# Performance work log

Measured on AMD Instinct MI355X. Metric: run time of the kernel, lower is better.

The kernel has to match this reference:

```python
import jax, jax.numpy as jnp
import numpy as np
from jax import lax

BS = 64    # block size
NH = 8     # attention heads
L = 12     # layers
NEG = -1e9
EPS = 1e-12  # BigBird layer_norm_eps


def gelu_new(x):
    c = 0.7978845608028654  # sqrt(2/pi)
    return 0.5 * x * (1.0 + jnp.tanh(c * (x + 0.044715 * x * x * x)))


def layer_norm(x, s, b):
    m = jnp.mean(x, axis=-1, keepdims=True)
    v = jnp.var(x, axis=-1, keepdims=True)
    return (x - m) * lax.rsqrt(v + EPS) * s + b


def block_sparse_attn(q, k, v, mask, key_blocks):
    # q,k,v: [B,H,S,hd]; mask: [B,S] (1=keep); key_blocks: [nb-2, K] block ids
    B, H, S, hd = q.shape
    nb = S // BS
    nm = nb - 2
    K = key_blocks.shape[1]
    scale = 1.0 / np.sqrt(hd)
    qb = q.reshape(B, H, nb, BS, hd)
    kb = k.reshape(B, H, nb, BS, hd)
    vb = v.reshape(B, H, nb, BS, hd)
    mb = mask.reshape(B, nb, BS)
    # middle query blocks: attend to gathered global+window+random key blocks
    q_mid = qb[:, :, 1:-1]                                   # [B,H,nm,BS,hd]
    kg = kb[:, :, key_blocks]                                # [B,H,nm,K,BS,hd]
    vg = vb[:, :, key_blocks].reshape(B, H, nm, K * BS, hd)
    mg = mb[:, key_blocks].reshape(B, 1, nm, 1, K * BS)
    s_mid = jnp.einsum('bhnqd,bhnkzd->bhnqkz', q_mid, kg).reshape(B, H, nm, BS, K * BS)
    s_mid = s_mid * scale + NEG * (1.0 - mg)
    ctx_mid = jnp.einsum('bhnqk,bhnkd->bhnqd', jax.nn.softmax(s_mid, axis=-1), vg)
    # first/last query blocks are global: full attention rows
    q_edge = jnp.stack([qb[:, :, 0], qb[:, :, -1]], axis=2)  # [B,H,2,BS,hd]
    s_edge = jnp.einsum('bhnqd,bhkd->bhnqk', q_edge, k) * scale
    s_edge = s_edge + NEG * (1.0 - mask)[:, None, None, None, :]
    ctx_edge = jnp.einsum('bhnqk,bhkd->bhnqd', jax.nn.softmax(s_edge, axis=-1), v)
    ctx = jnp.concatenate([ctx_edge[:, :, :1], ctx_mid, ctx_edge[:, :, 1:]], axis=2)
    return ctx.reshape(B, H, S, hd)


def encoder_layer(x, p, mask, key_blocks):
    Wq, bq, Wk, bk, Wv, bv, Wo, bo, l1s, l1b, Wi_, bi_, Wo2_, bo2_, l2s, l2b = p
    B, S, Hm = x.shape
    hd = Hm // NH
    def heads(t):
        return t.reshape(B, S, NH, hd).transpose(0, 2, 1, 3)
    q = heads(x @ Wq + bq)
    k = heads(x @ Wk + bk)
    v = heads(x @ Wv + bv)
    ctx = block_sparse_attn(q, k, v, mask, key_blocks)
    ctx = ctx.transpose(0, 2, 1, 3).reshape(B, S, Hm)
    x = layer_norm(x + ctx @ Wo + bo, l1s, l1b)
    ff = gelu_new(x @ Wi_ + bi_) @ Wo2_ + bo2_
    return layer_norm(x + ff, l2s, l2b)


def forward(x, proj_w, proj_b, pos_emb, tok_emb, emb_ln_s, emb_ln_b, Wq, bq, Wk, bk, Wv, bv, Wo, bo, ln1_s, ln1_b, Wi, bi, Wo2, bo2, ln2_s, ln2_b, cw1, cb1, cw2, cb2, mask, key_blocks):
    h = x @ proj_w + proj_b                 # input projection to hidden 1536
    h = h + pos_emb[None] + tok_emb         # BigBird embeddings (token_type id 0)
    h = layer_norm(h, emb_ln_s, emb_ln_b)
    stack = (Wq, bq, Wk, bk, Wv, bv, Wo, bo, ln1_s, ln1_b, Wi, bi, Wo2, bo2, ln2_s, ln2_b)
    def body(carry, p):
        return encoder_layer(carry, p, mask, key_blocks), None
    h, _ = lax.scan(jax.checkpoint(body), h, stack)
    # replaced classifier head applied per token: Linear->ReLU->Linear
    return jnp.maximum(h @ cw1 + cb1, 0.0) @ cw2 + cb2


def setup_inputs():
    key = jax.random.key(0)
    ks = iter(jax.random.split(key, 64))
    def w(*shape):
        return jax.random.normal(next(ks), shape, jnp.float32) * 0.02
    B, S, DIN, H, FF, T = 1, 4096, 1280, 1536, 3072, 256
    nb = S // BS
    # deterministic random-block plan: per middle block, 3 random blocks
    # outside {global 0, global nb-1, window i-1..i+1}
    rng = np.random.RandomState(0)
    rows = []
    for i in range(1, nb - 1):
        fixed = [0, nb - 1, i - 1, i, i + 1]
        cand = np.setdiff1d(np.arange(nb), np.array(fixed))
        rows.append(fixed + list(rng.choice(cand, 3, replace=False)))
    key_blocks = jnp.asarray(np.array(rows, dtype=np.int32))
    z = jnp.zeros
    o = jnp.ones
    return dict(
        x=jax.random.normal(next(ks), (B, S, DIN), jnp.float32),
        proj_w=w(DIN, H), proj_b=z((H,)),
        pos_emb=w(S, H), tok_emb=w(H),
        emb_ln_s=o((H,)), emb_ln_b=z((H,)),
        Wq=w(L, H, H), bq=z((L, H)), Wk=w(L, H, H), bk=z((L, H)),
        Wv=w(L, H, H), bv=z((L, H)), Wo=w(L, H, H), bo=z((L, H)),
        ln1_s=o((L, H)), ln1_b=z((L, H)),
        Wi=w(L, H, FF), bi=z((L, FF)), Wo2=w(L, FF, H), bo2=z((L, H)),
        ln2_s=o((L, H)), ln2_b=z((L, H)),
        cw1=w(H, 512), cb1=z((512,)), cw2=w(512, T), cb2=z((T,)),
        attention_mask=jnp.ones((B, S), jnp.int32),
        key_blocks=key_blocks)


def reference(x, proj_w, proj_b, pos_emb, tok_emb, emb_ln_s, emb_ln_b, Wq, bq, Wk, bk, Wv, bv, Wo, bo, ln1_s, ln1_b, Wi, bi, Wo2, bo2, ln2_s, ln2_b, cw1, cb1, cw2, cb2, attention_mask, key_blocks):
    mask = attention_mask.astype(jnp.float32)
    return forward(x, proj_w, proj_b, pos_emb, tok_emb, emb_ln_s, emb_ln_b, Wq, bq, Wk, bk, Wv, bv, Wo, bo, ln1_s, ln1_b, Wi, bi, Wo2, bo2, ln2_s, ln2_b, cw1, cb1, cw2, cb2, mask, key_blocks)
```

## Files before the change

kernel.cpp:

```cpp
#include <hip/hip_runtime.h>

typedef unsigned short u16;
typedef unsigned int u32;
typedef __bf16 bf16x8 __attribute__((ext_vector_type(8)));
typedef float f32x4 __attribute__((ext_vector_type(4)));

#define SEQ 4096
#define HM 1536
#define QKVN 4608

__device__ inline u16 f2b(float f){
  u32 u = __builtin_bit_cast(u32, f);
  return (u16)((u + 0x7fffu + ((u>>16)&1u)) >> 16);
}
__device__ inline bf16x8 ld8(const u16* p){ return *reinterpret_cast<const bf16x8*>(p); }
__device__ inline void gload16(const void* g, void* l){
  __builtin_amdgcn_global_load_lds((const __attribute__((address_space(1))) void*)g,
                                   (__attribute__((address_space(3))) void*)l, 16, 0, 0);
}

__global__ void cvt_k(const float* __restrict__ in, u16* __restrict__ outp, int n4){
  int i = blockIdx.x*256 + threadIdx.x;
  if (i < n4){
    float4 f = reinterpret_cast<const float4*>(in)[i];
    ushort4 u; u.x=f2b(f.x); u.y=f2b(f.y); u.z=f2b(f.z); u.w=f2b(f.w);
    reinterpret_cast<ushort4*>(outp)[i] = u;
  }
}

__global__ void tconv(const float* __restrict__ W, u16* __restrict__ Wt, int K, int N){
  __shared__ float tile[32][33];
  int n0 = blockIdx.x*32, k0 = blockIdx.y*32;
  int tx = threadIdx.x, ty = threadIdx.y;
  #pragma unroll
  for (int i=0;i<4;i++){
    int kk = ty + i*8;
    tile[kk][tx] = W[(size_t)(k0+kk)*N + n0 + tx];
  }
  __syncthreads();
  #pragma unroll
  for (int i=0;i<4;i++){
    int nn = ty + i*8;
    Wt[(size_t)(n0+nn)*K + k0 + tx] = f2b(tile[tx][nn]);
  }
}

__global__ void tconv3(const float* __restrict__ W0, const float* __restrict__ W1,
                       const float* __restrict__ W2, u16* __restrict__ Wt){
  __shared__ float tile[32][33];
  const float* W = (blockIdx.z==0) ? W0 : (blockIdx.z==1 ? W1 : W2);
  u16* dst = Wt + (size_t)blockIdx.z*1536*1536;
  int n0 = blockIdx.x*32, k0 = blockIdx.y*32;
  int tx = threadIdx.x, ty = threadIdx.y;
  #pragma unroll
  for (int i=0;i<4;i++){
    int kk = ty + i*8;
    tile[kk][tx] = W[(size_t)(k0+kk)*1536 + n0 + tx];
  }
  __syncthreads();
  #pragma unroll
  for (int i=0;i<4;i++){
    int nn = ty + i*8;
    dst[(size_t)(n0+nn)*1536 + k0 + tx] = f2b(tile[tx][nn]);
  }
}

__global__ void vtrans_k(const u16* __restrict__ qkv, u16* __restrict__ vt){
  __shared__ u16 tile[32][33];
  int c0 = blockIdx.x*32, s0 = blockIdx.y*32;
  int tx = threadIdx.x, ty = threadIdx.y;
  #pragma unroll
  for (int i=0;i<4;i++)
    tile[ty+i*8][tx] = qkv[(size_t)(s0+ty+i*8)*QKVN + 3072 + c0 + tx];
  __syncthreads();
  #pragma unroll
  for (int i=0;i<4;i++)
    vt[(size_t)(c0+ty+i*8)*SEQ + s0 + tx] = tile[tx][ty+i*8];
}

__global__ void concat3_k(float* __restrict__ dst, const float* __restrict__ a,
                          const float* __restrict__ b, const float* __restrict__ c){
  int i = blockIdx.x*256 + threadIdx.x;
  if (i < 1536){ dst[i]=a[i]; dst[1536+i]=b[i]; dst[3072+i]=c[i]; }
}

template<int MODE>
__global__ __launch_bounds__(256) void gemm_k(
                       const u16* __restrict__ A, const u16* __restrict__ Bt,
                       const float* __restrict__ bias, const float* __restrict__ resid,
                       const float* __restrict__ pos, const float* __restrict__ tok,
                       u16* __restrict__ outB, float* __restrict__ outF,
                       int M, int N, int K){
  __shared__ __align__(16) u16 As[128*32];
  __shared__ __align__(16) u16 Bs[128*32];
  const int t = threadIdx.x;
  const int m0 = blockIdx.y*128, n0 = blockIdx.x*128;
  const int w = t>>6, l = t&63;
  const int wm = (w>>1)*64, wn = (w&1)*64;
  const int lr = l&15, lg = l>>4;
  const int srow = w*32 + (l>>2);
  const int scol = (l&3)*8;
  const u16* Ap = A  + (size_t)(m0 + srow)*K + scol;
  const u16* Bp = Bt + (size_t)(n0 + srow)*K + scol;
  f32x4 acc[4][4] = {};

  for (int k0 = 0; k0 < K; k0 += 32){
    #pragma unroll
    for (int i=0;i<2;i++){
      gload16(Ap + (size_t)i*16*K + k0, &As[(w*2+i)*512]);
      gload16(Bp + (size_t)i*16*K + k0, &Bs[(w*2+i)*512]);
    }
    __syncthreads();
    bf16x8 af[4], bfr[4];
    #pragma unroll
    for (int i=0;i<4;i++){
      af[i]  = ld8(&As[(wm + i*16 + lr)*32 + lg*8]);
      bfr[i] = ld8(&Bs[(wn + i*16 + lr)*32 + lg*8]);
    }
    #pragma unroll
    for (int i=0;i<4;i++)
      #pragma unroll
      for (int j=0;j<4;j++)
        acc[i][j] = __builtin_amdgcn_mfma_f32_16x16x32_bf16(af[i], bfr[j], acc[i][j], 0,0,0);
    __syncthreads();
  }

  #pragma unroll
  for (int i=0;i<4;i++){
    #pragma unroll
    for (int j=0;j<4;j++){
      int col = n0 + wn + j*16 + lr;
      float bv = bias[col];
      #pragma unroll
      for (int r2=0;r2<4;r2++){
        int row = m0 + wm + i*16 + lg*4 + r2;
        float v = acc[i][j][r2] + bv;
        size_t idx = (size_t)row*N + col;
        if (MODE==0) outB[idx] = f2b(v);
        else if (MODE==1) outF[idx] = v + resid[idx];
        else if (MODE==2){
          float g = 0.5f*v*(1.f + tanhf(0.7978845608028654f*(v + 0.044715f*v*v*v)));
          outB[idx] = f2b(g);
        }
        else if (MODE==3) outB[idx] = f2b(fmaxf(v, 0.f));
        else if (MODE==4) outF[idx] = v;
        else if (MODE==5) outF[idx] = v + pos[idx] + tok[col];
      }
    }
  }
}

__global__ void ln_k(const float* __restrict__ in, const float* __restrict__ g,
                     const float* __restrict__ bta, float* __restrict__ xf,
                     u16* __restrict__ xb){
  const int row = blockIdx.x, t = threadIdx.x;
  const float2* rp = reinterpret_cast<const float2*>(in + (size_t)row*HM);
  float2 v[3]; float s=0.f, s2=0.f;
  #pragma unroll
  for (int i=0;i<3;i++){
    v[i] = rp[t + i*256];
    s += v[i].x + v[i].y; s2 += v[i].x*v[i].x + v[i].y*v[i].y;
  }
  #pragma unroll
  for (int o=32;o;o>>=1){ s += __shfl_down(s,o,64); s2 += __shfl_down(s2,o,64); }
  __shared__ float red[8];
  if ((t&63)==0){ red[t>>6]=s; red[4+(t>>6)]=s2; }
  __syncthreads();
  s = red[0]+red[1]+red[2]+red[3]; s2 = red[4]+red[5]+red[6]+red[7];
  float mean = s*(1.f/1536.f);
  float var  = s2*(1.f/1536.f) - mean*mean;
  float inv  = rsqrtf(var + 1e-12f);
  float2* xfp = reinterpret_cast<float2*>(xf + (size_t)row*HM);
  u32*    xbp = reinterpret_cast<u32*>(xb + (size_t)row*HM);
  #pragma unroll
  for (int i=0;i<3;i++){
    int c2 = t + i*256;
    float2 gg = reinterpret_cast<const float2*>(g)[c2];
    float2 bb = reinterpret_cast<const float2*>(bta)[c2];
    float y0 = (v[i].x-mean)*inv*gg.x + bb.x;
    float y1 = (v[i].y-mean)*inv*gg.y + bb.y;
    xfp[c2] = make_float2(y0, y1);
    xbp[c2] = (u32)f2b(y0) | ((u32)f2b(y1) << 16);
  }
}

__device__ inline int sp_off(int row, int colu16){
  return row*256 + ((((colu16)*2) ^ ((row&7)<<4)) >> 1);
}

__global__ __launch_bounds__(256, 2) void attn_k(
    const u16* __restrict__ qkv, const u16* __restrict__ vt,
    const int* __restrict__ kblocks, const int* __restrict__ amask,
    u16* __restrict__ ctx, float* __restrict__ pO,
    float* __restrict__ pm, float* __restrict__ pl){
  __shared__ __align__(16) u16 sQ[64][200];
  __shared__ __align__(16) u16 sP[64*256];
  __shared__ float swm[4][64];
  __shared__ float swl[4][64];
  __shared__ float s_m[64];
  __shared__ float s_l[64];
  __shared__ float s_al[64];

  const int t = threadIdx.x, w = t>>6, l = t&63;
  const int lr = l&15, lg = l>>4;
  const int b = blockIdx.x;
  int h, qb, split;
  bool partial;
  if (b < 496){ h = b/62; qb = 1 + b%62; split = 0; partial = false; }
  else { int e = b-496; split = e&7; int idx = e>>3; h = idx>>1; qb = (idx&1)?63:0; partial = true; }

  {
    const u16* qg = qkv + (size_t)(qb*64)*QKVN + h*192;
    #pragma unroll
    for (int i=0;i<6;i++){
      int idx = t + i*256;
      int row = idx/24, c8 = idx%24;
      *reinterpret_cast<int4*>(&sQ[row][c8*8]) =
        *reinterpret_cast<const int4*>(qg + (size_t)row*QKVN + c8*8);
    }
  }
  if (t < 64){ s_m[t] = -3.0e38f; s_l[t] = 0.f; }
  __syncthreads();

  f32x4 accO[4][3] = {};
  const float scale = 0.07216878364870323f;

  for (int c = 0; c < 2; ++c){
    int kb4[4];
    #pragma unroll
    for (int idx=0;idx<4;idx++)
      kb4[idx] = partial ? (split*8 + c*4 + idx) : kblocks[(qb-1)*8 + c*4 + idx];
    const int kb = kb4[w];
    const u16* kp = qkv + (size_t)(kb*64)*QKVN + 1536 + h*192;
    f32x4 acc[4][4] = {};
    #pragma unroll
    for (int d0=0; d0<192; d0+=32){
      bf16x8 aq[4], bk_[4];
      #pragma unroll
      for (int i=0;i<4;i++)  aq[i]  = ld8(&sQ[i*16+lr][d0+lg*8]);
      #pragma unroll
      for (int jn=0;jn<4;jn++) bk_[jn] = ld8(kp + (size_t)(jn*16+lr)*QKVN + d0 + lg*8);
      #pragma unroll
      for (int i=0;i<4;i++)
        #pragma unroll
        for (int jn=0;jn<4;jn++)
          acc[i][jn] = __builtin_amdgcn_mfma_f32_16x16x32_bf16(aq[i], bk_[jn], acc[i][jn], 0,0,0);
    }
    bf16x8 bvx[8][3];
    #pragma unroll
    for (int ks=0; ks<8; ks++){
      const int sb = kb4[ks>>1]*64 + (ks&1)*32 + lg*8;
      #pragma unroll
      for (int jn=0;jn<3;jn++)
        bvx[ks][jn] = ld8(vt + (size_t)(h*192 + w*48 + jn*16 + lr)*SEQ + sb);
    }
    float mcol[4];
    #pragma unroll
    for (int jn=0;jn<4;jn++)
      mcol[jn] = -1e9f*(1.f - (float)amask[kb*64 + jn*16 + lr]);
    float rmax[4][4];
    #pragma unroll
    for (int i=0;i<4;i++)
      #pragma unroll
      for (int r2=0;r2<4;r2++){
        float mx = -3.0e38f;
        #pragma unroll
        for (int jn=0;jn<4;jn++){
          float sv = acc[i][jn][r2]*scale + mcol[jn];
          acc[i][jn][r2] = sv;
          mx = fmaxf(mx, sv);
        }
        #pragma unroll
        for (int o=1;o<16;o<<=1) mx = fmaxf(mx, __shfl_xor(mx, o, 64));
        rmax[i][r2] = mx;
      }
    if (lr == 0){
      #pragma unroll
      for (int i=0;i<4;i++)
        #pragma unroll
        for (int r2=0;r2<4;r2++)
          swm[w][i*16+lg*4+r2] = rmax[i][r2];
    }
    __syncthreads();
    if (t < 64){
      float mo = s_m[t];
      float mn = fmaxf(fmaxf(fmaxf(swm[0][t], swm[1][t]), fmaxf(swm[2][t], swm[3][t])), mo);
      s_al[t] = __expf(mo - mn);
      s_m[t]  = mn;
    }
    __syncthreads();
    #pragma unroll
    for (int i=0;i<4;i++)
      #pragma unroll
      for (int r2=0;r2<4;r2++){
        const int row = i*16 + lg*4 + r2;
        const float mrow = s_m[row];
        float ssum = 0.f;
        #pragma unroll
        for (int jn=0;jn<4;jn++){
          float p = __expf(acc[i][jn][r2] - mrow);
          ssum += p;
          sP[sp_off(row, w*64 + jn*16 + lr)] = f2b(p);
        }
        #pragma unroll
        for (int o=1;o<16;o<<=1) ssum += __shfl_xor(ssum, o, 64);
        if (lr == 0) swl[w][row] = ssum;
      }
    #pragma unroll
    for (int i=0;i<4;i++)
      #pragma unroll
      for (int r2=0;r2<4;r2++){
        float a = s_al[i*16+lg*4+r2];
        #pragma unroll
        for (int jn=0;jn<3;jn++) accO[i][jn][r2] *= a;
      }
    __syncthreads();
    if (t < 64)
      s_l[t] = s_l[t]*s_al[t] + swl[0][t]+swl[1][t]+swl[2][t]+swl[3][t];
    #pragma unroll
    for (int ks=0; ks<8; ks++){
      bf16x8 ap[4];
      #pragma unroll
      for (int i=0;i<4;i++) ap[i] = ld8(&sP[sp_off(i*16+lr, ks*32 + lg*8)]);
      #pragma unroll
      for (int i=0;i<4;i++)
        #pragma unroll
        for (int jn=0;jn<3;jn++)
          accO[i][jn] = __builtin_amdgcn_mfma_f32_16x16x32_bf16(ap[i], bvx[ks][jn], accO[i][jn], 0,0,0);
    }
  }
  __syncthreads();
  if (!partial){
    #pragma unroll
    for (int i=0;i<4;i++)
      #pragma unroll
      for (int r2=0;r2<4;r2++){
        const int row = i*16+lg*4+r2;
        const float inv = 1.f / s_l[row];
        #pragma unroll
        for (int jn=0;jn<3;jn++){
          const int col = h*192 + w*48 + jn*16 + lr;
          ctx[(size_t)(qb*64+row)*HM + col] = f2b(accO[i][jn][r2] * inv);
        }
      }
  } else {
    const int e = b - 496;
    #pragma unroll
    for (int i=0;i<4;i++)
      #pragma unroll
      for (int r2=0;r2<4;r2++){
        const int row = i*16+lg*4+r2;
        #pragma unroll
        for (int jn=0;jn<3;jn++){
          const int col = w*48 + jn*16 + lr;
          pO[((size_t)e*64 + row)*192 + col] = accO[i][jn][r2];
        }
      }
    if (t < 64){ pm[e*64 + t] = s_m[t]; pl[e*64 + t] = s_l[t]; }
  }
}

__global__ void attn_comb_k(const float* __restrict__ pO, const float* __restrict__ pm,
                            const float* __restrict__ pl, u16* __restrict__ ctx){
  const int b = blockIdx.x;
  const int h = b>>1, qb = (b&1)?63:0;
  const int t = threadIdx.x;
  __shared__ float sA[8][64];
  __shared__ float sInv[64];
  if (t < 64){
    float mv[8]; float M = -3.0e38f;
    #pragma unroll
    for (int s=0;s<8;s++){ mv[s] = pm[(b*8+s)*64 + t]; M = fmaxf(M, mv[s]); }
    float L = 0.f;
    #pragma unroll
    for (int s=0;s<8;s++){
      float a = __expf(mv[s]-M);
      sA[s][t] = a;
      L += pl[(b*8+s)*64 + t]*a;
    }
    sInv[t] = 1.f/L;
  }
  __syncthreads();
  #pragma unroll
  for (int i=0;i<48;i++){
    int idx = t + i*256;
    int row = idx/192, col = idx%192;
    float acc = 0.f;
    #pragma unroll
    for (int s=0;s<8;s++)
      acc += sA[s][row] * pO[((size_t)(b*8+s)*64 + row)*192 + col];
    ctx[(size_t)(qb*64+row)*HM + h*192 + col] = f2b(acc * sInv[row]);
  }
}

extern "C" void kernel_launch(void* const* d_in, const int* in_sizes, int n_in,
                              void* d_out, int out_size, void* d_ws, size_t ws_size,
                              hipStream_t stream){
  const float* x       = (const float*)d_in[0];
  const float* proj_w  = (const float*)d_in[1];
  const float* proj_b  = (const float*)d_in[2];
  const float* pos_emb = (const float*)d_in[3];
  const float* tok_emb = (const float*)d_in[4];
  const float* embs    = (const float*)d_in[5];
  const float* embb    = (const float*)d_in[6];
  const float* Wq  = (const float*)d_in[7];
  const float* bq  = (const float*)d_in[8];
  const float* Wk  = (const float*)d_in[9];
  const float* bk  = (const float*)d_in[10];
  const float* Wv  = (const float*)d_in[11];
  const float* bv  = (const float*)d_in[12];
  const float* Wo  = (const float*)d_in[13];
  const float* bo  = (const float*)d_in[14];
  const float* l1s = (const float*)d_in[15];
  const float* l1b = (const float*)d_in[16];
  const float* Wi  = (const float*)d_in[17];
  const float* bi  = (const float*)d_in[18];
  const float* Wo2 = (const float*)d_in[19];
  const float* bo2 = (const float*)d_in[20];
  const float* l2s = (const float*)d_in[21];
  const float* l2b = (const float*)d_in[22];
  const float* cw1 = (const float*)d_in[23];
  const float* cb1 = (const float*)d_in[24];
  const float* cw2 = (const float*)d_in[25];
  const float* cb2 = (const float*)d_in[26];
  const int* amask = (const int*)d_in[27];
  const int* kblk  = (const int*)d_in[28];
  float* out = (float*)d_out;

  char* base = (char*)d_ws;
  size_t off = 0;
  auto carve = [&](size_t bytes)->char*{
    char* p = base + off; off += (bytes + 255) & ~(size_t)255; return p;
  };
  float* xf32  = (float*)carve(4096ULL*1536*4);
  float* preln = (float*)carve(4096ULL*1536*4);
  u16*   xbf   = (u16*)  carve(4096ULL*1536*2);
  u16*   xinbf = (u16*)  carve(4096ULL*1280*2);
  u16*   qkv   = (u16*)  carve(4096ULL*4608*2);
  u16*   vt    = (u16*)  carve(1536ULL*4096*2);
  u16*   ctx   = (u16*)  carve(4096ULL*1536*2);
  u16*   ff1   = (u16*)  carve(4096ULL*3072*2);
  u16*   cls1  = (u16*)  carve(4096ULL*512*2);
  u16*   wt    = (u16*)  carve(4608ULL*1536*2);
  float* b3    = (float*)carve(4608ULL*4);
  float* pO    = (float*)carve(128ULL*64*192*4);
  float* pm    = (float*)carve(128ULL*64*4);
  float* pl    = (float*)carve(128ULL*64*4);
  if (off > ws_size) return;

  const dim3 tb32(32,8);

  cvt_k<<<5120, 256, 0, stream>>>(x, xinbf, 4096*1280/4);
  tconv<<<dim3(48,40), tb32, 0, stream>>>(proj_w, wt, 1280, 1536);
  gemm_k<5><<<dim3(12,32), 256, 0, stream>>>(xinbf, wt, proj_b, nullptr, pos_emb, tok_emb,
                                             nullptr, preln, 4096, 1536, 1280);
  ln_k<<<4096, 256, 0, stream>>>(preln, embs, embb, xf32, xbf);

  for (int l = 0; l < 12; ++l){
    const float* wq  = Wq  + (size_t)l*1536*1536;
    const float* wk  = Wk  + (size_t)l*1536*1536;
    const float* wv  = Wv  + (size_t)l*1536*1536;
    const float* wo  = Wo  + (size_t)l*1536*1536;
    const float* wi  = Wi  + (size_t)l*1536*3072;
    const float* wo2 = Wo2 + (size_t)l*3072*1536;
    const float* bql = bq  + (size_t)l*1536;
    const float* bkl = bk  + (size_t)l*1536;
    const float* bvl = bv  + (size_t)l*1536;
    const float* bol = bo  + (size_t)l*1536;
    const float* bil = bi  + (size_t)l*3072;
    const float* bo2l= bo2 + (size_t)l*1536;
    const float* g1  = l1s + (size_t)l*1536;
    const float* be1 = l1b + (size_t)l*1536;
    const float* g2  = l2s + (size_t)l*1536;
    const float* be2 = l2b + (size_t)l*1536;

    tconv3<<<dim3(48,48,3), tb32, 0, stream>>>(wq, wk, wv, wt);
    concat3_k<<<6, 256, 0, stream>>>(b3, bql, bkl, bvl);
    gemm_k<0><<<dim3(36,32), 256, 0, stream>>>(xbf, wt, b3, nullptr, nullptr, nullptr,
                                               qkv, nullptr, 4096, 4608, 1536);
    vtrans_k<<<dim3(48,128), tb32, 0, stream>>>(qkv, vt);

    attn_k<<<624, 256, 0, stream>>>(qkv, vt, kblk, amask, ctx, pO, pm, pl);
    attn_comb_k<<<16, 256, 0, stream>>>(pO, pm, pl, ctx);

    tconv<<<dim3(48,48), tb32, 0, stream>>>(wo, wt, 1536, 1536);
    gemm_k<1><<<dim3(12,32), 256, 0, stream>>>(ctx, wt, bol, xf32, nullptr, nullptr,
                                               nullptr, preln, 4096, 1536, 1536);
    ln_k<<<4096, 256, 0, stream>>>(preln, g1, be1, xf32, xbf);

    tconv<<<dim3(96,48), tb32, 0, stream>>>(wi, wt, 1536, 3072);
    gemm_k<2><<<dim3(24,32), 256, 0, stream>>>(xbf, wt, bil, nullptr, nullptr, nullptr,
                                               ff1, nullptr, 4096, 3072, 1536);
    tconv<<<dim3(48,96), tb32, 0, stream>>>(wo2, wt, 3072, 1536);
    gemm_k<1><<<dim3(12,32), 256, 0, stream>>>(ff1, wt, bo2l, xf32, nullptr, nullptr,
                                               nullptr, preln, 4096, 1536, 3072);
    ln_k<<<4096, 256, 0, stream>>>(preln, g2, be2, xf32, xbf);
  }

  tconv<<<dim3(16,48), tb32, 0, stream>>>(cw1, wt, 1536, 512);
  gemm_k<3><<<dim3(4,32), 256, 0, stream>>>(xbf, wt, cb1, nullptr, nullptr, nullptr,
                                            cls1, nullptr, 4096, 512, 1536);
  tconv<<<dim3(8,16), tb32, 0, stream>>>(cw2, wt, 512, 256);
  gemm_k<4><<<dim3(2,32), 256, 0, stream>>>(cls1, wt, cb2, nullptr, nullptr, nullptr,
                                            nullptr, out, 4096, 256, 512);

  (void)in_sizes; (void)n_in; (void)out_size;
}
```

Before: 6.104 ms.

## Fuse V transpose into QKV GEMM, move residual into LN, shrink attention LDS

The QKV GEMM epilogue now writes the V columns straight into the transposed vt buffer, so the separate vtrans kernel goes away. The residual add moves out of the output-projection GEMMs into the LayerNorm kernel, which reads a bf16 GEMM output plus the fp32 residual. This removes the fp32 preln buffer traffic but rounds the pre-residual sum to bf16. The attention kernel halves its P scratch in LDS and stages P in two halves with extra barriers so it can run 3 blocks per CU. V fragments are now loaded per k-step instead of being preloaded into registers.

```diff
diff --git a/kernel.cpp b/kernel.cpp
--- a/kernel.cpp
+++ b/kernel.cpp
@@ -13,6 +13,7 @@
   u32 u = __builtin_bit_cast(u32, f);
   return (u16)((u + 0x7fffu + ((u>>16)&1u)) >> 16);
 }
+__device__ inline float b2f(u16 h){ return __builtin_bit_cast(float, (u32)h << 16); }
 __device__ inline bf16x8 ld8(const u16* p){ return *reinterpret_cast<const bf16x8*>(p); }
 __device__ inline void gload16(const void* g, void* l){
   __builtin_amdgcn_global_load_lds((const __attribute__((address_space(1))) void*)g,
@@ -65,19 +66,6 @@
   }
 }
 
-__global__ void vtrans_k(const u16* __restrict__ qkv, u16* __restrict__ vt){
-  __shared__ u16 tile[32][33];
-  int c0 = blockIdx.x*32, s0 = blockIdx.y*32;
-  int tx = threadIdx.x, ty = threadIdx.y;
-  #pragma unroll
-  for (int i=0;i<4;i++)
-    tile[ty+i*8][tx] = qkv[(size_t)(s0+ty+i*8)*QKVN + 3072 + c0 + tx];
-  __syncthreads();
-  #pragma unroll
-  for (int i=0;i<4;i++)
-    vt[(size_t)(c0+ty+i*8)*SEQ + s0 + tx] = tile[tx][ty+i*8];
-}
-
 __global__ void concat3_k(float* __restrict__ dst, const float* __restrict__ a,
                           const float* __restrict__ b, const float* __restrict__ c){
   int i = blockIdx.x*256 + threadIdx.x;
@@ -87,8 +75,9 @@
 template<int MODE>
 __global__ __launch_bounds__(256) void gemm_k(
                        const u16* __restrict__ A, const u16* __restrict__ Bt,
-                       const float* __restrict__ bias, const float* __restrict__ resid,
+                       const float* __restrict__ bias,
                        const float* __restrict__ pos, const float* __restrict__ tok,
+                       u16* __restrict__ vtp,
                        u16* __restrict__ outB, float* __restrict__ outF,
                        int M, int N, int K){
   __shared__ __align__(16) u16 As[128*32];
@@ -131,13 +120,22 @@
     for (int j=0;j<4;j++){
       int col = n0 + wn + j*16 + lr;
       float bv = bias[col];
+      const int row0 = m0 + wm + i*16 + lg*4;
+      if (MODE==0 && col >= 3072){
+        ushort4 q;
+        q.x = f2b(acc[i][j][0] + bv);
+        q.y = f2b(acc[i][j][1] + bv);
+        q.z = f2b(acc[i][j][2] + bv);
+        q.w = f2b(acc[i][j][3] + bv);
+        *reinterpret_cast<ushort4*>(&vtp[(size_t)(col-3072)*SEQ + row0]) = q;
+        continue;
+      }
       #pragma unroll
       for (int r2=0;r2<4;r2++){
-        int row = m0 + wm + i*16 + lg*4 + r2;
+        int row = row0 + r2;
         float v = acc[i][j][r2] + bv;
         size_t idx = (size_t)row*N + col;
-        if (MODE==0) outB[idx] = f2b(v);
-        else if (MODE==1) outF[idx] = v + resid[idx];
+        if (MODE==0 || MODE==1) outB[idx] = f2b(v);
         else if (MODE==2){
           float g = 0.5f*v*(1.f + tanhf(0.7978845608028654f*(v + 0.044715f*v*v*v)));
           outB[idx] = f2b(g);
@@ -150,15 +148,22 @@
   }
 }
 
-__global__ void ln_k(const float* __restrict__ in, const float* __restrict__ g,
-                     const float* __restrict__ bta, float* __restrict__ xf,
-                     u16* __restrict__ xb){
+template<int RES>
+__global__ void ln_k(const float* __restrict__ in, const u16* __restrict__ ga,
+                     const float* __restrict__ g, const float* __restrict__ bta,
+                     float* __restrict__ xf, u16* __restrict__ xb){
   const int row = blockIdx.x, t = threadIdx.x;
   const float2* rp = reinterpret_cast<const float2*>(in + (size_t)row*HM);
+  const u32* gp = reinterpret_cast<const u32*>(ga + (size_t)row*HM);
   float2 v[3]; float s=0.f, s2=0.f;
   #pragma unroll
   for (int i=0;i<3;i++){
     v[i] = rp[t + i*256];
+    if (RES){
+      u32 gw = gp[t + i*256];
+      v[i].x += b2f((u16)(gw & 0xffff));
+      v[i].y += b2f((u16)(gw >> 16));
+    }
     s += v[i].x + v[i].y; s2 += v[i].x*v[i].x + v[i].y*v[i].y;
   }
   #pragma unroll
@@ -185,16 +190,16 @@
 }
 
 __device__ inline int sp_off(int row, int colu16){
-  return row*256 + ((((colu16)*2) ^ ((row&7)<<4)) >> 1);
-}
-
-__global__ __launch_bounds__(256, 2) void attn_k(
+  return row*128 + ((((colu16)*2) ^ ((row&7)<<4)) >> 1);
+}
+
+__global__ __launch_bounds__(256, 3) void attn_k(
     const u16* __restrict__ qkv, const u16* __restrict__ vt,
     const int* __restrict__ kblocks, const int* __restrict__ amask,
     u16* __restrict__ ctx, float* __restrict__ pO,
     float* __restrict__ pm, float* __restrict__ pl){
   __shared__ __align__(16) u16 sQ[64][200];
-  __shared__ __align__(16) u16 sP[64*256];
+  __shared__ __align__(16) u16 sP[64*128];
   __shared__ float swm[4][64];
   __shared__ float swl[4][64];
   __shared__ float s_m[64];
@@ -228,8 +233,8 @@
   for (int c = 0; c < 2; ++c){
     int kb4[4];
     #pragma unroll
-    for (int idx=0;idx<4;idx++)
-      kb4[idx] = partial ? (split*8 + c*4 + idx) : kblocks[(qb-1)*8 + c*4 + idx];
+    for (int i=0;i<4;i++)
+      kb4[i] = partial ? (split*8 + c*4 + i) : kblocks[(qb-1)*8 + c*4 + i];
     const int kb = kb4[w];
     const u16* kp = qkv + (size_t)(kb*64)*QKVN + 1536 + h*192;
     f32x4 acc[4][4] = {};
@@ -246,19 +251,10 @@
         for (int jn=0;jn<4;jn++)
           acc[i][jn] = __builtin_amdgcn_mfma_f32_16x16x32_bf16(aq[i], bk_[jn], acc[i][jn], 0,0,0);
     }
-    bf16x8 bvx[8][3];
-    #pragma unroll
-    for (int ks=0; ks<8; ks++){
-      const int sb = kb4[ks>>1]*64 + (ks&1)*32 + lg*8;
-      #pragma unroll
-      for (int jn=0;jn<3;jn++)
-        bvx[ks][jn] = ld8(vt + (size_t)(h*192 + w*48 + jn*16 + lr)*SEQ + sb);
-    }
     float mcol[4];
     #pragma unroll
     for (int jn=0;jn<4;jn++)
       mcol[jn] = -1e9f*(1.f - (float)amask[kb*64 + jn*16 + lr]);
-    float rmax[4][4];
     #pragma unroll
     for (int i=0;i<4;i++)
       #pragma unroll
@@ -272,15 +268,8 @@
         }
         #pragma unroll
         for (int o=1;o<16;o<<=1) mx = fmaxf(mx, __shfl_xor(mx, o, 64));
-        rmax[i][r2] = mx;
-      }
-    if (lr == 0){
-      #pragma unroll
-      for (int i=0;i<4;i++)
-        #pragma unroll
-        for (int r2=0;r2<4;r2++)
-          swm[w][i*16+lg*4+r2] = rmax[i][r2];
-    }
+        if (lr == 0) swm[w][i*16+lg*4+r2] = mx;
+      }
     __syncthreads();
     if (t < 64){
       float mo = s_m[t];
@@ -299,8 +288,8 @@
         #pragma unroll
         for (int jn=0;jn<4;jn++){
           float p = __expf(acc[i][jn][r2] - mrow);
+          acc[i][jn][r2] = p;
           ssum += p;
-          sP[sp_off(row, w*64 + jn*16 + lr)] = f2b(p);
         }
         #pragma unroll
         for (int o=1;o<16;o<<=1) ssum += __shfl_xor(ssum, o, 64);
@@ -317,19 +306,63 @@
     __syncthreads();
     if (t < 64)
       s_l[t] = s_l[t]*s_al[t] + swl[0][t]+swl[1][t]+swl[2][t]+swl[3][t];
-    #pragma unroll
-    for (int ks=0; ks<8; ks++){
-      bf16x8 ap[4];
+    if (w < 2){
+      #pragma unroll
+      for (int i=0;i<4;i++)
+        #pragma unroll
+        for (int r2=0;r2<4;r2++){
+          const int row = i*16 + lg*4 + r2;
+          #pragma unroll
+          for (int jn=0;jn<4;jn++)
+            sP[sp_off(row, w*64 + jn*16 + lr)] = f2b(acc[i][jn][r2]);
+        }
+    }
+    __syncthreads();
+    #pragma unroll
+    for (int ks=0; ks<4; ks++){
+      bf16x8 ap[4], bv_[3];
       #pragma unroll
       for (int i=0;i<4;i++) ap[i] = ld8(&sP[sp_off(i*16+lr, ks*32 + lg*8)]);
+      const int sb = kb4[ks>>1]*64 + (ks&1)*32 + lg*8;
+      #pragma unroll
+      for (int jn=0;jn<3;jn++)
+        bv_[jn] = ld8(vt + (size_t)(h*192 + w*48 + jn*16 + lr)*SEQ + sb);
       #pragma unroll
       for (int i=0;i<4;i++)
         #pragma unroll
         for (int jn=0;jn<3;jn++)
-          accO[i][jn] = __builtin_amdgcn_mfma_f32_16x16x32_bf16(ap[i], bvx[ks][jn], accO[i][jn], 0,0,0);
-    }
-  }
-  __syncthreads();
+          accO[i][jn] = __builtin_amdgcn_mfma_f32_16x16x32_bf16(ap[i], bv_[jn], accO[i][jn], 0,0,0);
+    }
+    __syncthreads();
+    if (w >= 2){
+      #pragma unroll
+      for (int i=0;i<4;i++)
+        #pragma unroll
+        for (int r2=0;r2<4;r2++){
+          const int row = i*16 + lg*4 + r2;
+          #pragma unroll
+          for (int jn=0;jn<4;jn++)
+            sP[sp_off(row, (w-2)*64 + jn*16 + lr)] = f2b(acc[i][jn][r2]);
+        }
+    }
+    __syncthreads();
+    #pragma unroll
+    for (int ks=4; ks<8; ks++){
+      bf16x8 ap[4], bv_[3];
+      #pragma unroll
+      for (int i=0;i<4;i++) ap[i] = ld8(&sP[sp_off(i*16+lr, (ks-4)*32 + lg*8)]);
+      const int sb = kb4[ks>>1]*64 + (ks&1)*32 + lg*8;
+      #pragma unroll
+      for (int jn=0;jn<3;jn++)
+        bv_[jn] = ld8(vt + (size_t)(h*192 + w*48 + jn*16 + lr)*SEQ + sb);
+      #pragma unroll
+      for (int i=0;i<4;i++)
+        #pragma unroll
+        for (int jn=0;jn<3;jn++)
+          accO[i][jn] = __builtin_amdgcn_mfma_f32_16x16x32_bf16(ap[i], bv_[jn], accO[i][jn], 0,0,0);
+    }
+    __syncthreads();
+  }
   if (!partial){
     #pragma unroll
     for (int i=0;i<4;i++)
@@ -362,21 +395,21 @@
 
 __global__ void attn_comb_k(const float* __restrict__ pO, const float* __restrict__ pm,
                             const float* __restrict__ pl, u16* __restrict__ ctx){
-  const int b = blockIdx.x;
-  const int h = b>>1, qb = (b&1)?63:0;
+  const int bidx = blockIdx.x;
+  const int h = bidx>>1, qb = (bidx&1)?63:0;
   const int t = threadIdx.x;
   __shared__ float sA[8][64];
   __shared__ float sInv[64];
   if (t < 64){
-    float mv[8]; float M = -3.0e38f;
-    #pragma unroll
-    for (int s=0;s<8;s++){ mv[s] = pm[(b*8+s)*64 + t]; M = fmaxf(M, mv[s]); }
+    float M = -3.0e38f;
+    #pragma unroll
+    for (int s=0;s<8;s++) M = fmaxf(M, pm[(bidx*8+s)*64 + t]);
     float L = 0.f;
     #pragma unroll
     for (int s=0;s<8;s++){
-      float a = __expf(mv[s]-M);
+      float a = __expf(pm[(bidx*8+s)*64 + t] - M);
       sA[s][t] = a;
-      L += pl[(b*8+s)*64 + t]*a;
+      L += pl[(bidx*8+s)*64 + t]*a;
     }
     sInv[t] = 1.f/L;
   }
@@ -388,7 +421,7 @@
     float acc = 0.f;
     #pragma unroll
     for (int s=0;s<8;s++)
-      acc += sA[s][row] * pO[((size_t)(b*8+s)*64 + row)*192 + col];
+      acc += sA[s][row] * pO[((size_t)(bidx*8+s)*64 + row)*192 + col];
     ctx[(size_t)(qb*64+row)*HM + h*192 + col] = f2b(acc * sInv[row]);
   }
 }
@@ -433,12 +466,12 @@
     char* p = base + off; off += (bytes + 255) & ~(size_t)255; return p;
   };
   float* xf32  = (float*)carve(4096ULL*1536*4);
-  float* preln = (float*)carve(4096ULL*1536*4);
   u16*   xbf   = (u16*)  carve(4096ULL*1536*2);
   u16*   xinbf = (u16*)  carve(4096ULL*1280*2);
   u16*   qkv   = (u16*)  carve(4096ULL*4608*2);
   u16*   vt    = (u16*)  carve(1536ULL*4096*2);
   u16*   ctx   = (u16*)  carve(4096ULL*1536*2);
+  u16*   go    = (u16*)  carve(4096ULL*1536*2);
   u16*   ff1   = (u16*)  carve(4096ULL*3072*2);
   u16*   cls1  = (u16*)  carve(4096ULL*512*2);
   u16*   wt    = (u16*)  carve(4608ULL*1536*2);
@@ -452,9 +485,9 @@
 
   cvt_k<<<5120, 256, 0, stream>>>(x, xinbf, 4096*1280/4);
   tconv<<<dim3(48,40), tb32, 0, stream>>>(proj_w, wt, 1280, 1536);
-  gemm_k<5><<<dim3(12,32), 256, 0, stream>>>(xinbf, wt, proj_b, nullptr, pos_emb, tok_emb,
-                                             nullptr, preln, 4096, 1536, 1280);
-  ln_k<<<4096, 256, 0, stream>>>(preln, embs, embb, xf32, xbf);
+  gemm_k<5><<<dim3(12,32), 256, 0, stream>>>(xinbf, wt, proj_b, pos_emb, tok_emb,
+                                             nullptr, nullptr, xf32, 4096, 1536, 1280);
+  ln_k<0><<<4096, 256, 0, stream>>>(xf32, xbf , embs, embb, xf32, xbf);
 
   for (int l = 0; l < 12; ++l){
     const float* wq  = Wq  + (size_t)l*1536*1536;
@@ -476,33 +509,32 @@
 
     tconv3<<<dim3(48,48,3), tb32, 0, stream>>>(wq, wk, wv, wt);
     concat3_k<<<6, 256, 0, stream>>>(b3, bql, bkl, bvl);
-    gemm_k<0><<<dim3(36,32), 256, 0, stream>>>(xbf, wt, b3, nullptr, nullptr, nullptr,
-                                               qkv, nullptr, 4096, 4608, 1536);
-    vtrans_k<<<dim3(48,128), tb32, 0, stream>>>(qkv, vt);
+    gemm_k<0><<<dim3(36,32), 256, 0, stream>>>(xbf, wt, b3, nullptr, nullptr,
+                                               vt, qkv, nullptr, 4096, 4608, 1536);
 
     attn_k<<<624, 256, 0, stream>>>(qkv, vt, kblk, amask, ctx, pO, pm, pl);
     attn_comb_k<<<16, 256, 0, stream>>>(pO, pm, pl, ctx);
 
     tconv<<<dim3(48,48), tb32, 0, stream>>>(wo, wt, 1536, 1536);
-    gemm_k<1><<<dim3(12,32), 256, 0, stream>>>(ctx, wt, bol, xf32, nullptr, nullptr,
-                                               nullptr, preln, 4096, 1536, 1536);
-    ln_k<<<4096, 256, 0, stream>>>(preln, g1, be1, xf32, xbf);
+    gemm_k<1><<<dim3(12,32), 256, 0, stream>>>(ctx, wt, bol, nullptr, nullptr,
+                                               nullptr, go, nullptr, 4096, 1536, 1536);
+    ln_k<1><<<4096, 256, 0, stream>>>(xf32, go, g1, be1, xf32, xbf);
 
     tconv<<<dim3(96,48), tb32, 0, stream>>>(wi, wt, 1536, 3072);
-    gemm_k<2><<<dim3(24,32), 256, 0, stream>>>(xbf, wt, bil, nullptr, nullptr, nullptr,
-                                               ff1, nullptr, 4096, 3072, 1536);
+    gemm_k<2><<<dim3(24,32), 256, 0, stream>>>(xbf, wt, bil, nullptr, nullptr,
+                                               nullptr, ff1, nullptr, 4096, 3072, 1536);
     tconv<<<dim3(48,96), tb32, 0, stream>>>(wo2, wt, 3072, 1536);
-    gemm_k<1><<<dim3(12,32), 256, 0, stream>>>(ff1, wt, bo2l, xf32, nullptr, nullptr,
-                                               nullptr, preln, 4096, 1536, 3072);
-    ln_k<<<4096, 256, 0, stream>>>(preln, g2, be2, xf32, xbf);
+    gemm_k<1><<<dim3(12,32), 256, 0, stream>>>(ff1, wt, bo2l, nullptr, nullptr,
+                                               nullptr, go, nullptr, 4096, 1536, 3072);
+    ln_k<1><<<4096, 256, 0, stream>>>(xf32, go, g2, be2, xf32, xbf);
   }
 
   tconv<<<dim3(16,48), tb32, 0, stream>>>(cw1, wt, 1536, 512);
-  gemm_k<3><<<dim3(4,32), 256, 0, stream>>>(xbf, wt, cb1, nullptr, nullptr, nullptr,
-                                            cls1, nullptr, 4096, 512, 1536);
+  gemm_k<3><<<dim3(4,32), 256, 0, stream>>>(xbf, wt, cb1, nullptr, nullptr,
+                                            nullptr, cls1, nullptr, 4096, 512, 1536);
   tconv<<<dim3(8,16), tb32, 0, stream>>>(cw2, wt, 512, 256);
-  gemm_k<4><<<dim3(2,32), 256, 0, stream>>>(cls1, wt, cb2, nullptr, nullptr, nullptr,
-                                            nullptr, out, 4096, 256, 512);
+  gemm_k<4><<<dim3(2,32), 256, 0, stream>>>(cls1, wt, cb2, nullptr, nullptr,
+                                            nullptr, nullptr, out, 4096, 256, 512);
 
   (void)in_sizes; (void)n_in; (void)out_size;
 }
```

Measured after the change: 6.438 ms. 1.05x slower.
